# Optimization experiments

Measured on AMD Instinct MI355X. Metric: run time of the kernel, lower is better.

The kernel has to match this reference:

```python
import jax, jax.numpy as jnp
import numpy as np

B, T, E, QKV, H = 2, 2048, 1024, 1024, 16
DH = QKV // H
R_LAYER = 2

def rmsnorm(x):
    eps = jnp.finfo(x.dtype).eps
    return x * jax.lax.rsqrt(jnp.mean(x * x, axis=-1, keepdims=True) + eps)

def w_norm(w, n):
    # scale whole matrix so its (unbiased) std matches n**-0.5
    std = jnp.std(w, ddof=1)
    return w * (n ** -0.5 / (std + 1e-8))

def rotary(x, cos, sin):
    d = x.shape[-1] // 2
    x1, x2 = x[..., :d], x[..., d:]
    return jnp.concatenate([x1 * cos + x2 * sin, -x1 * sin + x2 * cos], axis=-1)

def w_split(w):
    w_qkv = w[:3 * QKV]                               # (3*QKV, E)
    w_sw = w[3 * QKV:5 * QKV].reshape(2 * E, QKV)     # (2*E, QKV)
    w_out = w[5 * QKV:]                               # (E, E)
    return w_qkv, w_sw, w_out

def aft(x, w_qkv):
    qkv = rmsnorm(x) @ w_qkv.T                        # (B,T,3*QKV)
    q, k, v = jnp.split(qkv, 3, axis=-1)
    q, k = rmsnorm(q), rmsnorm(k)
    wexp = jnp.exp(k)
    kv_c = jnp.cumsum(wexp * v, axis=1)
    w_c = jnp.cumsum(wexp, axis=1)
    y = jax.nn.sigmoid(q) * kv_c / (w_c + 1e-6)
    return x, y

def tea(x, cos, sin, w_qkv):
    qkv = (rmsnorm(x) @ w_qkv.T).reshape(B, T, H, 3 * DH)
    q, k, v = jnp.split(qkv, 3, axis=-1)              # each (B,T,H,DH)
    q, k = rotary(q, cos, sin), rotary(k, cos, sin)
    q, k = rmsnorm(q), rmsnorm(k)
    q = q.transpose(0, 2, 1, 3)                       # (B,H,T,DH)
    k = k.transpose(0, 2, 1, 3)
    v = v.transpose(0, 2, 1, 3)
    scores = jnp.einsum('bhqd,bhkd->bhqk', q, k) * DH ** -0.5
    mask = jnp.tril(jnp.ones((T, T), dtype=bool))
    scores = jnp.where(mask, scores, -jnp.inf)
    att = jax.nn.softmax(scores, axis=-1)
    y = jnp.einsum('bhqk,bhkd->bhqd', att, v)
    return x, y.transpose(0, 2, 1, 3).reshape(B, T, QKV)

def swiglu(x, y, w_sw, w_out, ret_oa=True):
    uv = y @ w_sw.T                                   # (B,T,2*E)
    u, v = jnp.split(uv, 2, axis=-1)
    out = x + (u * jax.nn.silu(v)) @ w_out.T
    if not ret_oa:
        return out
    o = rmsnorm(u.reshape(B * T, -1))
    a = v.reshape(B * T, -1)
    oa = jax.nn.softmax((o.T @ a) * E ** -0.5, axis=-1)  # (E,E)
    return out, oa

def setup_inputs():
    key = jax.random.key(0)
    k1, k2 = jax.random.split(key)
    x = jax.random.normal(k1, (B, T, E), dtype=jnp.float32)
    s = 3 ** 0.5 * E ** -0.5
    w = jax.random.uniform(k2, (5 * QKV + E, E), dtype=jnp.float32, minval=-s, maxval=s)
    half = DH // 2
    inv_freq = 1.0 / (10000.0 ** (jnp.arange(half, dtype=jnp.float32) / half))
    freqs = jnp.outer(jnp.arange(T, dtype=jnp.float32), inv_freq)  # (T, half)
    cos = jnp.cos(freqs)[:, None, :]                  # (T,1,half) broadcasts over (B,T,H,half)
    sin = jnp.sin(freqs)[:, None, :]
    return {"x": x, "w": w, "cos": cos, "sin": sin}

def reference(x, w, cos, sin):
    for i in range(R_LAYER):
        w_qkv, w_sw, w_out = w_split(w)
        w_qkv = w_norm(w_qkv, E)
        w_sw = w_norm(w_sw, QKV)
        w_out = w_norm(w_out, E)
        if (i + 1) % 4 == 0:
            x, y = tea(x, cos, sin, w_qkv)
        else:
            x, y = aft(x, w_qkv)
        x, oa = swiglu(x, y, w_sw, w_out, ret_oa=True)
        # RetentionMechanism.forward: hypernetwork weight mixing
        wT = w_norm(w @ oa, 5 * QKV + E)
        w = wT * jax.nn.silu(w) + w
    w_qkv, w_sw, w_out = w_split(w)                   # note: no w_norm on final split (matches source)
    x, y = tea(x, cos, sin, w_qkv)
    return swiglu(x, y, w_sw, w_out, ret_oa=False)
```

## Files before the change

kernel.cpp:

```cpp
#include <hip/hip_runtime.h>
#include <hip/hip_bf16.h>
#include <math.h>

#define TPB 256

constexpr int Bc = 2, Tc = 2048, Ec = 1024, QKVc = 1024, Hc = 16, DHc = 64;
constexpr long BT = (long)Bc * Tc;
constexpr int WR = 5 * QKVc + Ec;
constexpr float F32_EPS = 1.1920928955078125e-07f;
constexpr int NCH = 32, CHL = Tc / NCH;

typedef __attribute__((ext_vector_type(8))) short short8;
typedef __attribute__((ext_vector_type(4))) float f32x4;

__device__ __forceinline__ unsigned short f2bu(float f) {
    union { __hip_bfloat16 h; unsigned short u; } c; c.h = __float2bfloat16(f); return c.u;
}
__device__ __forceinline__ float bu2f(unsigned short u) {
    union { __hip_bfloat16 h; unsigned short u; } c; c.u = u; return __bfloat162float(c.h);
}
__device__ __forceinline__ float ldval(const float* p) { return *p; }
__device__ __forceinline__ float ldval(const unsigned short* p) { return bu2f(*p); }

__device__ __forceinline__ void gload_lds16(const void* g, void* l) {
    __builtin_amdgcn_global_load_lds((const __attribute__((address_space(1))) void*)g,
                                     (__attribute__((address_space(3))) void*)l, 16, 0, 0);
}

__global__ void k_std_partial3(const float* __restrict__ w, float* __restrict__ out) {
    __shared__ float ls[TPB], lss[TPB];
    int seg = blockIdx.y;
    long base = (seg == 0) ? 0L : (seg == 1 ? 3072L * 1024 : 5120L * 1024);
    long n    = (seg == 0) ? 3072L * 1024 : (seg == 1 ? 2048L * 1024 : 1024L * 1024);
    const float* p = w + base;
    float s = 0.f, ss = 0.f;
    for (long i = (long)blockIdx.x * TPB + threadIdx.x; i < n; i += 256L * TPB) {
        float v = p[i]; s += v; ss += v * v;
    }
    ls[threadIdx.x] = s; lss[threadIdx.x] = ss; __syncthreads();
    for (int o = 128; o > 0; o >>= 1) {
        if (threadIdx.x < o) { ls[threadIdx.x] += ls[threadIdx.x + o]; lss[threadIdx.x] += lss[threadIdx.x + o]; }
        __syncthreads();
    }
    if (threadIdx.x == 0) { out[seg * 512 + blockIdx.x] = ls[0]; out[seg * 512 + 256 + blockIdx.x] = lss[0]; }
}

__global__ void k_std_final3(const float* __restrict__ part, float* __restrict__ scales) {
    __shared__ float ls[TPB], lss[TPB];
    for (int seg = 0; seg < 3; ++seg) {
        ls[threadIdx.x] = part[seg * 512 + threadIdx.x];
        lss[threadIdx.x] = part[seg * 512 + 256 + threadIdx.x];
        __syncthreads();
        for (int o = 128; o > 0; o >>= 1) {
            if (threadIdx.x < o) { ls[threadIdx.x] += ls[threadIdx.x + o]; lss[threadIdx.x] += lss[threadIdx.x + o]; }
            __syncthreads();
        }
        if (threadIdx.x == 0) {
            float n = (seg == 0) ? 3145728.0f : (seg == 1 ? 2097152.0f : 1048576.0f);
            float var = (lss[0] - ls[0] * ls[0] / n) / (n - 1.0f);
            scales[seg] = 0.03125f / (sqrtf(fmaxf(var, 0.0f)) + 1e-8f);
        }
        __syncthreads();
    }
}

__global__ void k_std_partial(const float* __restrict__ p, long n, float* __restrict__ out) {
    __shared__ float ls[TPB], lss[TPB];
    float s = 0.f, ss = 0.f;
    for (long i = (long)blockIdx.x * TPB + threadIdx.x; i < n; i += (long)gridDim.x * TPB) {
        float v = p[i]; s += v; ss += v * v;
    }
    ls[threadIdx.x] = s; lss[threadIdx.x] = ss; __syncthreads();
    for (int o = 128; o > 0; o >>= 1) {
        if (threadIdx.x < o) { ls[threadIdx.x] += ls[threadIdx.x + o]; lss[threadIdx.x] += lss[threadIdx.x + o]; }
        __syncthreads();
    }
    if (threadIdx.x == 0) { out[blockIdx.x] = ls[0]; out[gridDim.x + blockIdx.x] = lss[0]; }
}

__global__ void k_std_final(const float* __restrict__ part, float n, float rs, float* __restrict__ scale) {
    __shared__ float ls[TPB], lss[TPB];
    ls[threadIdx.x] = part[threadIdx.x];
    lss[threadIdx.x] = part[TPB + threadIdx.x];
    __syncthreads();
    for (int o = 128; o > 0; o >>= 1) {
        if (threadIdx.x < o) { ls[threadIdx.x] += ls[threadIdx.x + o]; lss[threadIdx.x] += lss[threadIdx.x + o]; }
        __syncthreads();
    }
    if (threadIdx.x == 0) {
        float var = (lss[0] - ls[0] * ls[0] / n) / (n - 1.0f);
        scale[0] = rs / (sqrtf(fmaxf(var, 0.0f)) + 1e-8f);
    }
}

__global__ void k_rms1024(const float* __restrict__ in, float* __restrict__ out, long ldin, long ldout) {
    __shared__ float red[TPB];
    long row = blockIdx.x;
    float4 v = *(const float4*)(in + row * ldin + threadIdx.x * 4);
    float ss = v.x * v.x + v.y * v.y + v.z * v.z + v.w * v.w;
    red[threadIdx.x] = ss; __syncthreads();
    for (int o = 128; o > 0; o >>= 1) {
        if (threadIdx.x < o) red[threadIdx.x] += red[threadIdx.x + o];
        __syncthreads();
    }
    float sc = rsqrtf(red[0] / 1024.0f + F32_EPS);
    float4 o4; o4.x = v.x * sc; o4.y = v.y * sc; o4.z = v.z * sc; o4.w = v.w * sc;
    *(float4*)(out + row * ldout + threadIdx.x * 4) = o4;
}

__global__ void k_rms_qk(float* __restrict__ qkv) {
    __shared__ float red[TPB];
    int bid = blockIdx.x;
    long row = bid >> 1; int half = bid & 1;
    float* p = qkv + row * 3072 + half * 1024;
    float4 v = *(const float4*)(p + threadIdx.x * 4);
    float ss = v.x * v.x + v.y * v.y + v.z * v.z + v.w * v.w;
    red[threadIdx.x] = ss; __syncthreads();
    for (int o = 128; o > 0; o >>= 1) {
        if (threadIdx.x < o) red[threadIdx.x] += red[threadIdx.x + o];
        __syncthreads();
    }
    float sc = rsqrtf(red[0] / 1024.0f + F32_EPS);
    float4 o4; o4.x = v.x * sc; o4.y = v.y * sc; o4.z = v.z * sc; o4.w = v.w * sc;
    *(float4*)(p + threadIdx.x * 4) = o4;
}

__global__ void k_rms1024b(const float* __restrict__ in, unsigned short* __restrict__ out, long ldin, long ldout) {
    __shared__ float red[TPB];
    long row = blockIdx.x;
    float4 v = *(const float4*)(in + row * ldin + threadIdx.x * 4);
    float ss = v.x * v.x + v.y * v.y + v.z * v.z + v.w * v.w;
    red[threadIdx.x] = ss; __syncthreads();
    for (int o = 128; o > 0; o >>= 1) {
        if (threadIdx.x < o) red[threadIdx.x] += red[threadIdx.x + o];
        __syncthreads();
    }
    float sc = rsqrtf(red[0] / 1024.0f + F32_EPS);
    ushort4 o4; o4.x = f2bu(v.x * sc); o4.y = f2bu(v.y * sc); o4.z = f2bu(v.z * sc); o4.w = f2bu(v.w * sc);
    *(ushort4*)(out + row * ldout + threadIdx.x * 4) = o4;
}

__global__ void k_cast_bf16(const float* __restrict__ in, unsigned short* __restrict__ out, long n4) {
    long i = (long)blockIdx.x * TPB + threadIdx.x;
    if (i >= n4) return;
    float4 v = *(const float4*)(in + i * 4);
    ushort4 o; o.x = f2bu(v.x); o.y = f2bu(v.y); o.z = f2bu(v.z); o.w = f2bu(v.w);
    *(ushort4*)(out + i * 4) = o;
}

template<typename TI>
__global__ void k_tcast(const TI* __restrict__ in, long ldi, long sIn,
                        unsigned short* __restrict__ out, long ldo, long sOut,
                        const float* __restrict__ rowscale) {
    __shared__ float tile[64][65];
    const TI* ip = in + (long)blockIdx.z * sIn;
    unsigned short* op = out + (long)blockIdx.z * sOut;
    int r0 = blockIdx.y * 64, c0 = blockIdx.x * 64;
    int tid = threadIdx.x;
    int rr = tid >> 4, cc = (tid & 15) * 4;
    #pragma unroll
    for (int u = 0; u < 4; ++u) {
        int r = rr + u * 16;
        float sc = rowscale ? rowscale[r0 + r] : 1.0f;
        #pragma unroll
        for (int j = 0; j < 4; ++j)
            tile[r][cc + j] = ldval(ip + (long)(r0 + r) * ldi + c0 + cc + j) * sc;
    }
    __syncthreads();
    #pragma unroll
    for (int u = 0; u < 4; ++u) {
        int c = rr + u * 16;
        ushort4 o;
        o.x = f2bu(tile[cc + 0][c]); o.y = f2bu(tile[cc + 1][c]);
        o.z = f2bu(tile[cc + 2][c]); o.w = f2bu(tile[cc + 3][c]);
        *(ushort4*)(op + (long)(c0 + c) * ldo + r0 + cc) = o;
    }
}

__global__ void k_tcast2(const float* __restrict__ uv, const float* __restrict__ uscale,
                         unsigned short* __restrict__ t1, unsigned short* __restrict__ t2) {
    __shared__ float tile[64][65];
    int z = blockIdx.z;
    const float* ip = uv + (z ? 1024 : 0);
    unsigned short* op = z ? t2 : t1;
    int r0 = blockIdx.y * 64, c0 = blockIdx.x * 64;
    int tid = threadIdx.x;
    int rr = tid >> 4, cc = (tid & 15) * 4;
    #pragma unroll
    for (int u = 0; u < 4; ++u) {
        int r = rr + u * 16;
        float sc = z ? 1.0f : uscale[r0 + r];
        #pragma unroll
        for (int j = 0; j < 4; ++j)
            tile[r][cc + j] = ip[(long)(r0 + r) * 2048 + c0 + cc + j] * sc;
    }
    __syncthreads();
    #pragma unroll
    for (int u = 0; u < 4; ++u) {
        int c = rr + u * 16;
        ushort4 o;
        o.x = f2bu(tile[cc + 0][c]); o.y = f2bu(tile[cc + 1][c]);
        o.z = f2bu(tile[cc + 2][c]); o.w = f2bu(tile[cc + 3][c]);
        *(ushort4*)(op + (long)(c0 + c) * 4096 + r0 + cc) = o;
    }
}

template<int WGM, int WGN, int WRITE_BF16>
__global__ __launch_bounds__(256)
void k_bgemm(int K,
             const unsigned short* __restrict__ A, int lda, long sA,
             const unsigned short* __restrict__ B, int ldb, long sB,
             void* __restrict__ C, int ldc, long sCi, long sSplit, int nsplit,
             const float* __restrict__ scale_ptr, float fscale,
             const float* __restrict__ addp, int ldadd) {
    constexpr int TM = WGM * 64, TN = WGN * 64;
    __shared__ unsigned short Asl[TM * 32];
    __shared__ unsigned short Bsl[TN * 32];
    int bz = blockIdx.z;
    int batch = bz, sp = 0;
    if (nsplit > 1) { batch = bz / nsplit; sp = bz - batch * nsplit; }
    int m0 = blockIdx.y * TM, n0 = blockIdx.x * TN;
    const unsigned short* Ap = A + (long)batch * sA + (long)sp * K;
    const unsigned short* Bp = B + (long)batch * sB + (long)sp * K;
    int tid = threadIdx.x, lane = tid & 63, wave = tid >> 6;
    int wr = wave / WGN, wc = wave % WGN;
    f32x4 acc[4][4] = {};
    constexpr int CAW = TM / 64;
    constexpr int CBW = TN / 64;
    for (int k0 = 0; k0 < K; k0 += 32) {
        #pragma unroll
        for (int c = 0; c < CAW; ++c) {
            int bu = (wave * CAW + c) * 64;
            int uidx = bu + lane;
            int r = uidx >> 2, slot = uidx & 3;
            int gu = slot ^ ((r >> 1) & 3);
            gload_lds16(Ap + (long)(m0 + r) * lda + k0 + gu * 8, Asl + bu * 8);
        }
        #pragma unroll
        for (int c = 0; c < CBW; ++c) {
            int bu = (wave * CBW + c) * 64;
            int uidx = bu + lane;
            int r = uidx >> 2, slot = uidx & 3;
            int gu = slot ^ ((r >> 1) & 3);
            gload_lds16(Bp + (long)(n0 + r) * ldb + k0 + gu * 8, Bsl + bu * 8);
        }
        __syncthreads();
        short8 av[4], bv[4];
        #pragma unroll
        for (int m = 0; m < 4; ++m) {
            int r = wr * 64 + m * 16 + (lane & 15);
            int slot = (lane >> 4) ^ ((r >> 1) & 3);
            av[m] = *(const short8*)(Asl + r * 32 + slot * 8);
        }
        #pragma unroll
        for (int n = 0; n < 4; ++n) {
            int r = wc * 64 + n * 16 + (lane & 15);
            int slot = (lane >> 4) ^ ((r >> 1) & 3);
            bv[n] = *(const short8*)(Bsl + r * 32 + slot * 8);
        }
        #pragma unroll
        for (int m = 0; m < 4; ++m)
            #pragma unroll
            for (int n = 0; n < 4; ++n)
                acc[m][n] = __builtin_amdgcn_mfma_f32_16x16x32_bf16(av[m], bv[n], acc[m][n], 0, 0, 0);
        __syncthreads();
    }
    float s = fscale * (scale_ptr ? scale_ptr[0] : 1.0f);
    long cbase = (long)batch * sCi + (long)sp * sSplit;
    int row0 = m0 + wr * 64, col0 = n0 + wc * 64 + (lane & 15);
    int rbase = (lane >> 4) * 4;
    #pragma unroll
    for (int m = 0; m < 4; ++m)
        #pragma unroll
        for (int i = 0; i < 4; ++i) {
            long row = row0 + m * 16 + rbase + i;
            #pragma unroll
            for (int n = 0; n < 4; ++n) {
                long col = col0 + n * 16;
                float v = acc[m][n][i] * s;
                if (addp) v += addp[row * (long)ldadd + col];
                long idx = cbase + row * ldc + col;
                if (WRITE_BF16) ((unsigned short*)C)[idx] = f2bu(v);
                else ((float*)C)[idx] = v;
            }
        }
}

__global__ __launch_bounds__(64)
void k_flash_split(const unsigned short* __restrict__ hq, const unsigned short* __restrict__ hk,
                   const unsigned short* __restrict__ hvT,
                   float* __restrict__ opart, float* __restrict__ mpart, float* __restrict__ lpart) {
    __shared__ unsigned short P[32 * 72];
    int lane = threadIdx.x;
    int g = lane >> 4, c = lane & 15;
    unsigned bid = blockIdx.x;
    unsigned swz = (bid & 7) * 640 + (bid >> 3);
    unsigned bh = swz / 160, itr = swz % 160;
    int item = 159 - (int)itr;
    int strip, chunk;
    if (item < 16)      { strip = item;                 chunk = 0; }
    else if (item < 48) { strip = 16 + (item - 16) / 2; chunk = (item - 16) & 1; }
    else if (item < 96) { strip = 32 + (item - 48) / 3; chunk = (item - 48) % 3; }
    else                { strip = 48 + (item - 96) / 4; chunk = (item - 96) & 3; }
    int q0 = strip * 32;
    int nt = (q0 + 32 + 63) >> 6;
    int ti0 = chunk * 8;
    int ti1 = ti0 + 8 < nt ? ti0 + 8 : nt;
    const unsigned short* qb = hq + (long)bh * Tc * 64;
    const unsigned short* kb = hk + (long)bh * Tc * 64;
    const unsigned short* vtb = hvT + (long)bh * 64 * Tc;

    short8 qf[2][2];
    #pragma unroll
    for (int mf = 0; mf < 2; ++mf)
        #pragma unroll
        for (int ks = 0; ks < 2; ++ks)
            qf[mf][ks] = *(const short8*)(qb + (long)(q0 + mf * 16 + c) * 64 + ks * 32 + g * 8);

    f32x4 o_acc[2][4] = {};
    float m_run[2][4], l_run[2][4];
    #pragma unroll
    for (int mf = 0; mf < 2; ++mf)
        #pragma unroll
        for (int i = 0; i < 4; ++i) { m_run[mf][i] = -3.0e38f; l_run[mf][i] = 0.f; }

    for (int ti = ti0; ti < ti1; ++ti) {
        int kt = ti * 64;
        short8 vf[2][4];
        #pragma unroll
        for (int ks = 0; ks < 2; ++ks)
            #pragma unroll
            for (int df = 0; df < 4; ++df)
                vf[ks][df] = *(const short8*)(vtb + (long)(df * 16 + c) * Tc + kt + ks * 32 + g * 8);
        f32x4 s_acc[2][4] = {};
        #pragma unroll
        for (int ks = 0; ks < 2; ++ks) {
            short8 kf[4];
            #pragma unroll
            for (int nf = 0; nf < 4; ++nf)
                kf[nf] = *(const short8*)(kb + (long)(kt + nf * 16 + c) * 64 + ks * 32 + g * 8);
            #pragma unroll
            for (int mf = 0; mf < 2; ++mf)
                #pragma unroll
                for (int nf = 0; nf < 4; ++nf)
                    s_acc[mf][nf] = __builtin_amdgcn_mfma_f32_16x16x32_bf16(qf[mf][ks], kf[nf], s_acc[mf][nf], 0, 0, 0);
        }
        bool diag = (kt + 64 > q0);
        #pragma unroll
        for (int mf = 0; mf < 2; ++mf)
            #pragma unroll
            for (int nf = 0; nf < 4; ++nf)
                #pragma unroll
                for (int i = 0; i < 4; ++i) {
                    float v = s_acc[mf][nf][i] * 0.125f;
                    if (diag && (kt + nf * 16 + c) > (q0 + mf * 16 + g * 4 + i)) v = -3.0e38f;
                    s_acc[mf][nf][i] = v;
                }
        float pm[2][4];
        #pragma unroll
        for (int mf = 0; mf < 2; ++mf)
            #pragma unroll
            for (int i = 0; i < 4; ++i)
                pm[mf][i] = fmaxf(fmaxf(s_acc[mf][0][i], s_acc[mf][1][i]),
                                  fmaxf(s_acc[mf][2][i], s_acc[mf][3][i]));
        #pragma unroll
        for (int lvl = 1; lvl <= 8; lvl <<= 1)
            #pragma unroll
            for (int mf = 0; mf < 2; ++mf)
                #pragma unroll
                for (int i = 0; i < 4; ++i)
                    pm[mf][i] = fmaxf(pm[mf][i], __shfl_xor(pm[mf][i], lvl));
        float corr[2][4], ls[2][4];
        #pragma unroll
        for (int mf = 0; mf < 2; ++mf)
            #pragma unroll
            for (int i = 0; i < 4; ++i) {
                float mn = fmaxf(m_run[mf][i], pm[mf][i]);
                corr[mf][i] = __expf(m_run[mf][i] - mn);
                m_run[mf][i] = mn;
                ls[mf][i] = 0.f;
            }
        #pragma unroll
        for (int mf = 0; mf < 2; ++mf)
            #pragma unroll
            for (int nf = 0; nf < 4; ++nf)
                #pragma unroll
                for (int i = 0; i < 4; ++i) {
                    float p = __expf(s_acc[mf][nf][i] - m_run[mf][i]);
                    unsigned short pb = f2bu(p);
                    P[(mf * 16 + g * 4 + i) * 72 + nf * 16 + c] = pb;
                    ls[mf][i] += bu2f(pb);
                }
        #pragma unroll
        for (int lvl = 1; lvl <= 8; lvl <<= 1)
            #pragma unroll
            for (int mf = 0; mf < 2; ++mf)
                #pragma unroll
                for (int i = 0; i < 4; ++i)
                    ls[mf][i] += __shfl_xor(ls[mf][i], lvl);
        #pragma unroll
        for (int mf = 0; mf < 2; ++mf)
            #pragma unroll
            for (int i = 0; i < 4; ++i) {
                l_run[mf][i] = l_run[mf][i] * corr[mf][i] + ls[mf][i];
                #pragma unroll
                for (int df = 0; df < 4; ++df) o_acc[mf][df][i] *= corr[mf][i];
            }
        #pragma unroll
        for (int ks = 0; ks < 2; ++ks) {
            short8 pa[2];
            #pragma unroll
            for (int mf = 0; mf < 2; ++mf)
                pa[mf] = *(const short8*)(P + (mf * 16 + c) * 72 + ks * 32 + g * 8);
            #pragma unroll
            for (int mf = 0; mf < 2; ++mf)
                #pragma unroll
                for (int df = 0; df < 4; ++df)
                    o_acc[mf][df] = __builtin_amdgcn_mfma_f32_16x16x32_bf16(pa[mf], vf[ks][df], o_acc[mf][df], 0, 0, 0);
        }
    }
    long pbase = (long)(bh * 160 + item);
    #pragma unroll
    for (int mf = 0; mf < 2; ++mf)
        #pragma unroll
        for (int i = 0; i < 4; ++i) {
            int row_l = mf * 16 + g * 4 + i;
            #pragma unroll
            for (int df = 0; df < 4; ++df)
                opart[pbase * 2048 + row_l * 64 + df * 16 + c] = o_acc[mf][df][i];
            if (c == 0) {
                mpart[pbase * 32 + row_l] = m_run[mf][i];
                lpart[pbase * 32 + row_l] = l_run[mf][i];
            }
        }
}

__global__ __launch_bounds__(256)
void k_flash_merge(const float* __restrict__ opart, const float* __restrict__ mpart,
                   const float* __restrict__ lpart, unsigned short* __restrict__ yout) {
    int bs = blockIdx.x;
    int bh = bs >> 6, strip = bs & 63;
    int b = bh >> 4, h = bh & 15;
    int np, base;
    if (strip < 16)      { np = 1; base = strip; }
    else if (strip < 32) { np = 2; base = 16 + (strip - 16) * 2; }
    else if (strip < 48) { np = 3; base = 48 + (strip - 32) * 3; }
    else                 { np = 4; base = 96 + (strip - 48) * 4; }
    long p0 = (long)(bh * 160 + base);
    int tid = threadIdx.x;
    int r = tid >> 3, c0 = (tid & 7) * 8;
    float M = -3.0e38f;
    for (int p = 0; p < np; ++p) M = fmaxf(M, mpart[(p0 + p) * 32 + r]);
    float L = 0.f;
    float acc[8] = {};
    for (int p = 0; p < np; ++p) {
        float sc = __expf(mpart[(p0 + p) * 32 + r] - M);
        L += lpart[(p0 + p) * 32 + r] * sc;
        const float* op = opart + (p0 + p) * 2048 + r * 64 + c0;
        #pragma unroll
        for (int j = 0; j < 8; ++j) acc[j] += op[j] * sc;
    }
    float inv = 1.0f / L;
    long row = (long)b * Tc + strip * 32 + r;
    unsigned short* yp = yout + row * 1024 + h * 64 + c0;
    ushort4 o1, o2;
    o1.x = f2bu(acc[0] * inv); o1.y = f2bu(acc[1] * inv); o1.z = f2bu(acc[2] * inv); o1.w = f2bu(acc[3] * inv);
    o2.x = f2bu(acc[4] * inv); o2.y = f2bu(acc[5] * inv); o2.z = f2bu(acc[6] * inv); o2.w = f2bu(acc[7] * inv);
    *(ushort4*)yp = o1;
    *(ushort4*)(yp + 4) = o2;
}

__global__ void k_aft_p1(const float* __restrict__ qkv, float* __restrict__ cw, float* __restrict__ cs) {
    int id = blockIdx.x * TPB + threadIdx.x;
    int bc = id & 2047, ch = id >> 11;
    int b = bc >> 10, c = bc & 1023;
    const float* base = qkv + ((long)(b * Tc + ch * CHL)) * 3072 + c;
    float sw = 0.f, sv = 0.f;
    for (int i = 0; i < CHL; ++i) {
        float k = base[1024], v = base[2048];
        float e = __expf(k);
        sw += e; sv += e * v;
        base += 3072;
    }
    cw[ch * 2048 + bc] = sw; cs[ch * 2048 + bc] = sv;
}

__global__ void k_aft_p3(const float* __restrict__ qkv, const float* __restrict__ cw,
                         const float* __restrict__ cs, unsigned short* __restrict__ y) {
    int id = blockIdx.x * TPB + threadIdx.x;
    int bc = id & 2047, ch = id >> 11;
    int b = bc >> 10, c = bc & 1023;
    float aw = 0.f, av = 0.f;
    for (int cc = 0; cc < ch; ++cc) { aw += cw[cc * 2048 + bc]; av += cs[cc * 2048 + bc]; }
    long t0 = (long)b * Tc + ch * CHL;
    const float* base = qkv + t0 * 3072 + c;
    unsigned short* yp = y + t0 * 1024 + c;
    for (int i = 0; i < CHL; ++i) {
        float q = base[0], k = base[1024], v = base[2048];
        float e = __expf(k);
        av += e * v; aw += e;
        float sig = 1.0f / (1.0f + __expf(-q));
        yp[0] = f2bu(sig * av / (aw + 1e-6f));
        base += 3072; yp += 1024;
    }
}

__global__ void k_silu_rms(const float* __restrict__ uv, unsigned short* __restrict__ g,
                           float* __restrict__ rs) {
    __shared__ float red[TPB];
    long row = blockIdx.x;
    const float* up = uv + row * 2048;
    float4 u = *(const float4*)(up + threadIdx.x * 4);
    float4 v = *(const float4*)(up + 1024 + threadIdx.x * 4);
    ushort4 o;
    o.x = f2bu(u.x * v.x / (1.f + __expf(-v.x)));
    o.y = f2bu(u.y * v.y / (1.f + __expf(-v.y)));
    o.z = f2bu(u.z * v.z / (1.f + __expf(-v.z)));
    o.w = f2bu(u.w * v.w / (1.f + __expf(-v.w)));
    *(ushort4*)(g + row * 1024 + threadIdx.x * 4) = o;
    red[threadIdx.x] = u.x * u.x + u.y * u.y + u.z * u.z + u.w * u.w;
    __syncthreads();
    for (int off = 128; off > 0; off >>= 1) {
        if (threadIdx.x < off) red[threadIdx.x] += red[threadIdx.x + off];
        __syncthreads();
    }
    if (threadIdx.x == 0) rs[row] = rsqrtf(red[0] / 1024.0f + F32_EPS);
}

__global__ void k_silu_gate(const float* __restrict__ uv, unsigned short* __restrict__ g, long n4) {
    long i = (long)blockIdx.x * TPB + threadIdx.x;
    if (i >= n4) return;
    long r = i >> 8, c4 = i & 255;
    float4 u = *(const float4*)(uv + r * 2048 + c4 * 4);
    float4 v = *(const float4*)(uv + r * 2048 + 1024 + c4 * 4);
    ushort4 o;
    o.x = f2bu(u.x * v.x / (1.f + __expf(-v.x)));
    o.y = f2bu(u.y * v.y / (1.f + __expf(-v.y)));
    o.z = f2bu(u.z * v.z / (1.f + __expf(-v.z)));
    o.w = f2bu(u.w * v.w / (1.f + __expf(-v.w)));
    *(ushort4*)(g + r * 1024 + c4 * 4) = o;
}

__global__ void k_wupdate(float* __restrict__ w, const float* __restrict__ p,
                          const float* __restrict__ scale, unsigned short* __restrict__ wb, long n4) {
    long i = (long)blockIdx.x * TPB + threadIdx.x;
    if (i >= n4) return;
    float s = scale[0];
    float4 wv = *(const float4*)(w + i * 4);
    float4 pv = *(const float4*)(p + i * 4);
    float4 o;
    o.x = pv.x * s * (wv.x / (1.f + __expf(-wv.x))) + wv.x;
    o.y = pv.y * s * (wv.y / (1.f + __expf(-wv.y))) + wv.y;
    o.z = pv.z * s * (wv.z / (1.f + __expf(-wv.z))) + wv.z;
    o.w = pv.w * s * (wv.w / (1.f + __expf(-wv.w))) + wv.w;
    *(float4*)(w + i * 4) = o;
    ushort4 ob; ob.x = f2bu(o.x); ob.y = f2bu(o.y); ob.z = f2bu(o.z); ob.w = f2bu(o.w);
    *(ushort4*)(wb + i * 4) = ob;
}

__global__ void k_softmax4(const float* __restrict__ parts, float* __restrict__ outb, float fscale) {
    __shared__ float red[TPB];
    __shared__ float rowbuf[1024];
    long row = blockIdx.x;
    const float* p0 = parts + row * 1024;
    for (int c = threadIdx.x; c < 1024; c += TPB) {
        float v = p0[c] + p0[c + 1048576] + p0[c + 2097152] + p0[c + 3145728];
        rowbuf[c] = v * fscale;
    }
    __syncthreads();
    float m = -3.0e38f;
    for (int c = threadIdx.x; c < 1024; c += TPB) m = fmaxf(m, rowbuf[c]);
    red[threadIdx.x] = m; __syncthreads();
    for (int o = 128; o > 0; o >>= 1) {
        if (threadIdx.x < o) red[threadIdx.x] = fmaxf(red[threadIdx.x], red[threadIdx.x + o]);
        __syncthreads();
    }
    m = red[0]; __syncthreads();
    float sum = 0.f;
    for (int c = threadIdx.x; c < 1024; c += TPB) sum += __expf(rowbuf[c] - m);
    red[threadIdx.x] = sum; __syncthreads();
    for (int o = 128; o > 0; o >>= 1) {
        if (threadIdx.x < o) red[threadIdx.x] += red[threadIdx.x + o];
        __syncthreads();
    }
    float inv = 1.0f / red[0];
    for (int c = threadIdx.x; c < 1024; c += TPB)
        outb[row * 1024 + c] = __expf(rowbuf[c] - m) * inv;
}

__global__ void k_rot_split(const float* __restrict__ qkvp, const float* __restrict__ cosp,
                            const float* __restrict__ sinp, unsigned short* __restrict__ hq,
                            unsigned short* __restrict__ hk, unsigned short* __restrict__ hv) {
    __shared__ float row[3072];
    __shared__ float cs[32], sn[32];
    int bt = blockIdx.x;
    int b = bt >> 11, t = bt & 2047;
    const float* src = qkvp + (long)bt * 3072;
    #pragma unroll
    for (int u = 0; u < 3; ++u) {
        int idx = threadIdx.x + u * 256;
        *(float4*)&row[idx * 4] = *(const float4*)(src + idx * 4);
    }
    if (threadIdx.x < 32) { cs[threadIdx.x] = cosp[t * 32 + threadIdx.x]; sn[threadIdx.x] = sinp[t * 32 + threadIdx.x]; }
    __syncthreads();
    int h = threadIdx.x >> 4, li = threadIdx.x & 15;
    int base = h * 192;
    long obase = ((long)(b * Hc + h) * Tc + t) * 64 + li * 4;
    {
        float r[4]; float ss = 0.f;
        #pragma unroll
        for (int j = 0; j < 4; ++j) {
            int d = li * 4 + j;
            float val = (d < 32) ? (row[base + d] * cs[d] + row[base + d + 32] * sn[d])
                                 : (-row[base + d - 32] * sn[d - 32] + row[base + d] * cs[d - 32]);
            r[j] = val; ss += val * val;
        }
        ss += __shfl_xor(ss, 1); ss += __shfl_xor(ss, 2); ss += __shfl_xor(ss, 4); ss += __shfl_xor(ss, 8);
        float sc = rsqrtf(ss / 64.0f + F32_EPS);
        ushort4 o; o.x = f2bu(r[0] * sc); o.y = f2bu(r[1] * sc); o.z = f2bu(r[2] * sc); o.w = f2bu(r[3] * sc);
        *(ushort4*)(hq + obase) = o;
    }
    {
        int kb = base + 64;
        float r[4]; float ss = 0.f;
        #pragma unroll
        for (int j = 0; j < 4; ++j) {
            int d = li * 4 + j;
            float val = (d < 32) ? (row[kb + d] * cs[d] + row[kb + d + 32] * sn[d])
                                 : (-row[kb + d - 32] * sn[d - 32] + row[kb + d] * cs[d - 32]);
            r[j] = val; ss += val * val;
        }
        ss += __shfl_xor(ss, 1); ss += __shfl_xor(ss, 2); ss += __shfl_xor(ss, 4); ss += __shfl_xor(ss, 8);
        float sc = rsqrtf(ss / 64.0f + F32_EPS);
        ushort4 o; o.x = f2bu(r[0] * sc); o.y = f2bu(r[1] * sc); o.z = f2bu(r[2] * sc); o.w = f2bu(r[3] * sc);
        *(ushort4*)(hk + obase) = o;
    }
    {
        ushort4 o;
        o.x = f2bu(row[base + 128 + li * 4 + 0]); o.y = f2bu(row[base + 128 + li * 4 + 1]);
        o.z = f2bu(row[base + 128 + li * 4 + 2]); o.w = f2bu(row[base + 128 + li * 4 + 3]);
        *(ushort4*)(hv + obase) = o;
    }
}

extern "C" void kernel_launch(void* const* d_in, const int* in_sizes, int n_in,
                              void* d_out, int out_size, void* d_ws, size_t ws_size,
                              hipStream_t stream) {
    const float* x_in = (const float*)d_in[0];
    const float* w_in = (const float*)d_in[1];
    const float* cos_in = (const float*)d_in[2];
    const float* sin_in = (const float*)d_in[3];
    float* out = (float*)d_out;
    float* ws = (float*)d_ws;

    long off = 0;
    float* w_cur = ws + off;  off += (long)WR * Ec;
    float* w_tmp = ws + off;  off += (long)WR * Ec;
    float* xbuf  = ws + off;  off += BT * Ec;
    float* qkv   = ws + off;  off += BT * 3L * QKVc;
    float* oab   = ws + off;  off += (long)Ec * Ec;
    float* red   = ws + off;  off += 2048;
    float* scales= ws + off;  off += 16;
    float* uscale= ws + off;  off += 4096;
    float* chw   = ws + off;  off += 2048L * NCH;
    float* chs   = ws + off;  off += 2048L * NCH;
    float* uv    = qkv;
    float* opart = qkv;
    float* mpart = oab;
    float* lpart = oab + 5120L * 32;

    unsigned short* bp = (unsigned short*)(ws + off);
    long bo = 0;
    unsigned short* wb  = bp + bo; bo += (long)WR * Ec;
    unsigned short* xbn = bp + bo; bo += BT * Ec;
    unsigned short* ybn = bp + bo; bo += BT * Ec;
    unsigned short* gbn = bp + bo; bo += BT * Ec;
    unsigned short* t1  = bp + bo; bo += BT * Ec;
    unsigned short* t2  = bp + bo; bo += BT * Ec;
    unsigned short* t3  = bp + bo; bo += BT * Ec;
    unsigned short* t4  = bp + bo; bo += BT * Ec;

    hipMemcpyAsync(w_cur, w_in, (size_t)WR * Ec * 4, hipMemcpyDeviceToDevice, stream);
    hipMemcpyAsync(xbuf, x_in, (size_t)BT * Ec * 4, hipMemcpyDeviceToDevice, stream);

    const float rsWR = 1.0f / sqrtf(6144.0f);
    const long wsw = 3072L * 1024, wout = 5120L * 1024;

    k_cast_bf16<<<(int)(((long)WR * Ec / 4) / TPB), TPB, 0, stream>>>(w_cur, wb, (long)WR * Ec / 4);

    for (int layer = 0; layer < 2; ++layer) {
        k_std_partial3<<<dim3(256, 3), TPB, 0, stream>>>(w_cur, red);
        k_std_final3<<<1, TPB, 0, stream>>>(red, scales);
        k_rms1024b<<<BT, TPB, 0, stream>>>(xbuf, xbn, 1024, 1024);
        k_bgemm<2, 2, 0><<<dim3(24, 32, 1), TPB, 0, stream>>>(
            1024, xbn, 1024, 0, wb, 1024, 0, qkv, 3072, 0, 0, 1, scales + 0, 1.0f, nullptr, 0);
        k_rms_qk<<<8192, TPB, 0, stream>>>(qkv);
        k_aft_p1<<<(2048 * NCH) / TPB, TPB, 0, stream>>>(qkv, chw, chs);
        k_aft_p3<<<(2048 * NCH) / TPB, TPB, 0, stream>>>(qkv, chw, chs, ybn);
        k_bgemm<2, 2, 0><<<dim3(16, 32, 1), TPB, 0, stream>>>(
            1024, ybn, 1024, 0, wb + wsw, 1024, 0, uv, 2048, 0, 0, 1, scales + 1, 1.0f, nullptr, 0);
        k_silu_rms<<<BT, TPB, 0, stream>>>(uv, gbn, uscale);
        k_tcast2<<<dim3(16, 64, 2), TPB, 0, stream>>>(uv, uscale, t1, t2);
        k_bgemm<2, 2, 0><<<dim3(8, 8, 4), TPB, 0, stream>>>(
            1024, t1, 4096, 0, t2, 4096, 0, w_tmp, 1024, 0, 1048576L, 4, nullptr, 1.0f, nullptr, 0);
        k_softmax4<<<1024, TPB, 0, stream>>>(w_tmp, oab, 0.03125f);
        k_tcast<float><<<dim3(16, 16, 1), TPB, 0, stream>>>(oab, 1024, 0, t3, 1024, 0, nullptr);
        k_bgemm<2, 2, 0><<<dim3(8, 32, 1), TPB, 0, stream>>>(
            1024, gbn, 1024, 0, wb + wout, 1024, 0, xbuf, 1024, 0, 0, 1, scales + 2, 1.0f, xbuf, 1024);
        k_bgemm<2, 2, 0><<<dim3(8, 48, 1), TPB, 0, stream>>>(
            1024, wb, 1024, 0, t3, 1024, 0, w_tmp, 1024, 0, 0, 1, nullptr, 1.0f, nullptr, 0);
        k_std_partial<<<256, TPB, 0, stream>>>(w_tmp, (long)WR * 1024, red);
        k_std_final<<<1, TPB, 0, stream>>>(red, (float)((long)WR * 1024), rsWR, scales + 3);
        k_wupdate<<<(int)(((long)WR * 1024 / 4) / TPB), TPB, 0, stream>>>(
            w_cur, w_tmp, scales + 3, wb, (long)WR * 1024 / 4);
    }

    k_rms1024b<<<BT, TPB, 0, stream>>>(xbuf, xbn, 1024, 1024);
    k_bgemm<2, 2, 0><<<dim3(24, 32, 1), TPB, 0, stream>>>(
        1024, xbn, 1024, 0, wb, 1024, 0, qkv, 3072, 0, 0, 1, nullptr, 1.0f, nullptr, 0);
    k_rot_split<<<BT, TPB, 0, stream>>>(qkv, cos_in, sin_in, t1, t2, t3);
    k_tcast<unsigned short><<<dim3(1, 32, 32), TPB, 0, stream>>>(
        t3, 64, (long)Tc * 64, t4, 2048, (long)Tc * 64, nullptr);
    k_flash_split<<<dim3(5120), 64, 0, stream>>>(t1, t2, t4, opart, mpart, lpart);
    k_flash_merge<<<dim3(2048), TPB, 0, stream>>>(opart, mpart, lpart, ybn);
    k_bgemm<2, 2, 0><<<dim3(16, 32, 1), TPB, 0, stream>>>(
        1024, ybn, 1024, 0, wb + wsw, 1024, 0, uv, 2048, 0, 0, 1, nullptr, 1.0f, nullptr, 0);
    k_silu_gate<<<(int)((BT * 1024 / 4) / TPB), TPB, 0, stream>>>(uv, gbn, BT * 1024 / 4);
    k_bgemm<2, 2, 0><<<dim3(8, 32, 1), TPB, 0, stream>>>(
        1024, gbn, 1024, 0, wb + wout, 1024, 0, out, 1024, 0, 0, 1, nullptr, 1.0f, xbuf, 1024);
}
```

Measured before the change: 879.7 us.

## Drop input copies, lazily rescale flash softmax, and double AFT chunk count

Measured after the change: 866.4 us. Within noise of the previous version (-1.5%).

```diff
diff --git a/kernel.cpp b/kernel.cpp
--- a/kernel.cpp
+++ b/kernel.cpp
@@ -8,7 +8,7 @@
 constexpr long BT = (long)Bc * Tc;
 constexpr int WR = 5 * QKVc + Ec;
 constexpr float F32_EPS = 1.1920928955078125e-07f;
-constexpr int NCH = 32, CHL = Tc / NCH;
+constexpr int NCH = 64, CHL = Tc / NCH;
 
 typedef __attribute__((ext_vector_type(8))) short short8;
 typedef __attribute__((ext_vector_type(4))) float f32x4;
@@ -91,21 +91,6 @@
         float var = (lss[0] - ls[0] * ls[0] / n) / (n - 1.0f);
         scale[0] = rs / (sqrtf(fmaxf(var, 0.0f)) + 1e-8f);
     }
-}
-
-__global__ void k_rms1024(const float* __restrict__ in, float* __restrict__ out, long ldin, long ldout) {
-    __shared__ float red[TPB];
-    long row = blockIdx.x;
-    float4 v = *(const float4*)(in + row * ldin + threadIdx.x * 4);
-    float ss = v.x * v.x + v.y * v.y + v.z * v.z + v.w * v.w;
-    red[threadIdx.x] = ss; __syncthreads();
-    for (int o = 128; o > 0; o >>= 1) {
-        if (threadIdx.x < o) red[threadIdx.x] += red[threadIdx.x + o];
-        __syncthreads();
-    }
-    float sc = rsqrtf(red[0] / 1024.0f + F32_EPS);
-    float4 o4; o4.x = v.x * sc; o4.y = v.y * sc; o4.z = v.z * sc; o4.w = v.w * sc;
-    *(float4*)(out + row * ldout + threadIdx.x * 4) = o4;
 }
 
 __global__ void k_rms_qk(float* __restrict__ qkv) {
@@ -318,11 +303,11 @@
             qf[mf][ks] = *(const short8*)(qb + (long)(q0 + mf * 16 + c) * 64 + ks * 32 + g * 8);
 
     f32x4 o_acc[2][4] = {};
-    float m_run[2][4], l_run[2][4];
+    float m_run[2][4], lpp[2][4];
     #pragma unroll
     for (int mf = 0; mf < 2; ++mf)
         #pragma unroll
-        for (int i = 0; i < 4; ++i) { m_run[mf][i] = -3.0e38f; l_run[mf][i] = 0.f; }
+        for (int i = 0; i < 4; ++i) { m_run[mf][i] = -3.0e38f; lpp[mf][i] = 0.f; }
 
     for (int ti = ti0; ti < ti1; ++ti) {
         int kt = ti * 64;
@@ -345,17 +330,15 @@
                 for (int nf = 0; nf < 4; ++nf)
                     s_acc[mf][nf] = __builtin_amdgcn_mfma_f32_16x16x32_bf16(qf[mf][ks], kf[nf], s_acc[mf][nf], 0, 0, 0);
         }
-        bool diag = (kt + 64 > q0);
-        #pragma unroll
-        for (int mf = 0; mf < 2; ++mf)
-            #pragma unroll
-            for (int nf = 0; nf < 4; ++nf)
+        if (ti == nt - 1) {
+            #pragma unroll
+            for (int mf = 0; mf < 2; ++mf)
                 #pragma unroll
-                for (int i = 0; i < 4; ++i) {
-                    float v = s_acc[mf][nf][i] * 0.125f;
-                    if (diag && (kt + nf * 16 + c) > (q0 + mf * 16 + g * 4 + i)) v = -3.0e38f;
-                    s_acc[mf][nf][i] = v;
-                }
+                for (int nf = 0; nf < 4; ++nf)
+                    #pragma unroll
+                    for (int i = 0; i < 4; ++i)
+                        if ((kt + nf * 16 + c) > (q0 + mf * 16 + g * 4 + i)) s_acc[mf][nf][i] = -1.0e30f;
+        }
         float pm[2][4];
         #pragma unroll
         for (int mf = 0; mf < 2; ++mf)
@@ -370,42 +353,37 @@
                 #pragma unroll
                 for (int i = 0; i < 4; ++i)
                     pm[mf][i] = fmaxf(pm[mf][i], __shfl_xor(pm[mf][i], lvl));
-        float corr[2][4], ls[2][4];
+        float mg = 0.f;
         #pragma unroll
         for (int mf = 0; mf < 2; ++mf)
             #pragma unroll
             for (int i = 0; i < 4; ++i) {
-                float mn = fmaxf(m_run[mf][i], pm[mf][i]);
-                corr[mf][i] = __expf(m_run[mf][i] - mn);
-                m_run[mf][i] = mn;
-                ls[mf][i] = 0.f;
+                pm[mf][i] *= 0.125f;
+                mg = fmaxf(mg, pm[mf][i] - m_run[mf][i]);
             }
+        if (__any(mg > 8.0f)) {
+            #pragma unroll
+            for (int mf = 0; mf < 2; ++mf)
+                #pragma unroll
+                for (int i = 0; i < 4; ++i) {
+                    float mn = fmaxf(m_run[mf][i], pm[mf][i]);
+                    float corr = __expf(m_run[mf][i] - mn);
+                    m_run[mf][i] = mn;
+                    lpp[mf][i] *= corr;
+                    #pragma unroll
+                    for (int df = 0; df < 4; ++df) o_acc[mf][df][i] *= corr;
+                }
+        }
         #pragma unroll
         for (int mf = 0; mf < 2; ++mf)
             #pragma unroll
             for (int nf = 0; nf < 4; ++nf)
                 #pragma unroll
                 for (int i = 0; i < 4; ++i) {
-                    float p = __expf(s_acc[mf][nf][i] - m_run[mf][i]);
-                    unsigned short pb = f2bu(p);
-                    P[(mf * 16 + g * 4 + i) * 72 + nf * 16 + c] = pb;
-                    ls[mf][i] += bu2f(pb);
+                    float p = __expf(fmaf(s_acc[mf][nf][i], 0.125f, -m_run[mf][i]));
+                    P[(mf * 16 + g * 4 + i) * 72 + nf * 16 + c] = f2bu(p);
+                    lpp[mf][i] += p;
                 }
-        #pragma unroll
-        for (int lvl = 1; lvl <= 8; lvl <<= 1)
-            #pragma unroll
-            for (int mf = 0; mf < 2; ++mf)
-                #pragma unroll
-                for (int i = 0; i < 4; ++i)
-                    ls[mf][i] += __shfl_xor(ls[mf][i], lvl);
-        #pragma unroll
-        for (int mf = 0; mf < 2; ++mf)
-            #pragma unroll
-            for (int i = 0; i < 4; ++i) {
-                l_run[mf][i] = l_run[mf][i] * corr[mf][i] + ls[mf][i];
-                #pragma unroll
-                for (int df = 0; df < 4; ++df) o_acc[mf][df][i] *= corr[mf][i];
-            }
         #pragma unroll
         for (int ks = 0; ks < 2; ++ks) {
             short8 pa[2];
@@ -419,6 +397,13 @@
                     o_acc[mf][df] = __builtin_amdgcn_mfma_f32_16x16x32_bf16(pa[mf], vf[ks][df], o_acc[mf][df], 0, 0, 0);
         }
     }
+    #pragma unroll
+    for (int lvl = 1; lvl <= 8; lvl <<= 1)
+        #pragma unroll
+        for (int mf = 0; mf < 2; ++mf)
+            #pragma unroll
+            for (int i = 0; i < 4; ++i)
+                lpp[mf][i] += __shfl_xor(lpp[mf][i], lvl);
     long pbase = (long)(bh * 160 + item);
     #pragma unroll
     for (int mf = 0; mf < 2; ++mf)
@@ -430,7 +415,7 @@
                 opart[pbase * 2048 + row_l * 64 + df * 16 + c] = o_acc[mf][df][i];
             if (c == 0) {
                 mpart[pbase * 32 + row_l] = m_run[mf][i];
-                lpart[pbase * 32 + row_l] = l_run[mf][i];
+                lpart[pbase * 32 + row_l] = lpp[mf][i];
             }
         }
 }
@@ -541,19 +526,20 @@
     *(ushort4*)(g + r * 1024 + c4 * 4) = o;
 }
 
-__global__ void k_wupdate(float* __restrict__ w, const float* __restrict__ p,
-                          const float* __restrict__ scale, unsigned short* __restrict__ wb, long n4) {
+__global__ void k_wupdate(float* __restrict__ wout, const float* __restrict__ win,
+                          const float* __restrict__ p, const float* __restrict__ scale,
+                          unsigned short* __restrict__ wb, long n4) {
     long i = (long)blockIdx.x * TPB + threadIdx.x;
     if (i >= n4) return;
     float s = scale[0];
-    float4 wv = *(const float4*)(w + i * 4);
+    float4 wv = *(const float4*)(win + i * 4);
     float4 pv = *(const float4*)(p + i * 4);
     float4 o;
     o.x = pv.x * s * (wv.x / (1.f + __expf(-wv.x))) + wv.x;
     o.y = pv.y * s * (wv.y / (1.f + __expf(-wv.y))) + wv.y;
     o.z = pv.z * s * (wv.z / (1.f + __expf(-wv.z))) + wv.z;
     o.w = pv.w * s * (wv.w / (1.f + __expf(-wv.w))) + wv.w;
-    *(float4*)(w + i * 4) = o;
+    *(float4*)(wout + i * 4) = o;
     ushort4 ob; ob.x = f2bu(o.x); ob.y = f2bu(o.y); ob.z = f2bu(o.z); ob.w = f2bu(o.w);
     *(ushort4*)(wb + i * 4) = ob;
 }
@@ -680,18 +666,17 @@
     unsigned short* t3  = bp + bo; bo += BT * Ec;
     unsigned short* t4  = bp + bo; bo += BT * Ec;
 
-    hipMemcpyAsync(w_cur, w_in, (size_t)WR * Ec * 4, hipMemcpyDeviceToDevice, stream);
-    hipMemcpyAsync(xbuf, x_in, (size_t)BT * Ec * 4, hipMemcpyDeviceToDevice, stream);
-
     const float rsWR = 1.0f / sqrtf(6144.0f);
     const long wsw = 3072L * 1024, wout = 5120L * 1024;
 
-    k_cast_bf16<<<(int)(((long)WR * Ec / 4) / TPB), TPB, 0, stream>>>(w_cur, wb, (long)WR * Ec / 4);
+    k_cast_bf16<<<(int)(((long)WR * Ec / 4) / TPB), TPB, 0, stream>>>(w_in, wb, (long)WR * Ec / 4);
 
     for (int layer = 0; layer < 2; ++layer) {
-        k_std_partial3<<<dim3(256, 3), TPB, 0, stream>>>(w_cur, red);
+        const float* wsrc = layer == 0 ? w_in : w_cur;
+        const float* xsrc = layer == 0 ? x_in : xbuf;
+        k_std_partial3<<<dim3(256, 3), TPB, 0, stream>>>(wsrc, red);
         k_std_final3<<<1, TPB, 0, stream>>>(red, scales);
-        k_rms1024b<<<BT, TPB, 0, stream>>>(xbuf, xbn, 1024, 1024);
+        k_rms1024b<<<BT, TPB, 0, stream>>>(xsrc, xbn, 1024, 1024);
         k_bgemm<2, 2, 0><<<dim3(24, 32, 1), TPB, 0, stream>>>(
             1024, xbn, 1024, 0, wb, 1024, 0, qkv, 3072, 0, 0, 1, scales + 0, 1.0f, nullptr, 0);
         k_rms_qk<<<8192, TPB, 0, stream>>>(qkv);
@@ -706,13 +691,13 @@
         k_softmax4<<<1024, TPB, 0, stream>>>(w_tmp, oab, 0.03125f);
         k_tcast<float><<<dim3(16, 16, 1), TPB, 0, stream>>>(oab, 1024, 0, t3, 1024, 0, nullptr);
         k_bgemm<2, 2, 0><<<dim3(8, 32, 1), TPB, 0, stream>>>(
-            1024, gbn, 1024, 0, wb + wout, 1024, 0, xbuf, 1024, 0, 0, 1, scales + 2, 1.0f, xbuf, 1024);
+            1024, gbn, 1024, 0, wb + wout, 1024, 0, xbuf, 1024, 0, 0, 1, scales + 2, 1.0f, xsrc, 1024);
         k_bgemm<2, 2, 0><<<dim3(8, 48, 1), TPB, 0, stream>>>(
             1024, wb, 1024, 0, t3, 1024, 0, w_tmp, 1024, 0, 0, 1, nullptr, 1.0f, nullptr, 0);
         k_std_partial<<<256, TPB, 0, stream>>>(w_tmp, (long)WR * 1024, red);
         k_std_final<<<1, TPB, 0, stream>>>(red, (float)((long)WR * 1024), rsWR, scales + 3);
         k_wupdate<<<(int)(((long)WR * 1024 / 4) / TPB), TPB, 0, stream>>>(
-            w_cur, w_tmp, scales + 3, wb, (long)WR * 1024 / 4);
+            w_cur, wsrc, w_tmp, scales + 3, wb, (long)WR * 1024 / 4);
     }
 
     k_rms1024b<<<BT, TPB, 0, stream>>>(xbuf, xbn, 1024, 1024);
```
